# Kernel optimization log

Measured on AMD Instinct MI355X. Metric: run time of the kernel, lower is better.

The kernel has to match this reference:

```python
import jax, jax.numpy as jnp
import numpy as np

B, S, H = 32, 4096, 512


def setup_inputs() -> dict:
    key = jax.random.key(0)
    k1, k2, k3, k4, k5 = jax.random.split(key, 5)
    scale = 1.0 / np.sqrt(H)
    return {
        "query": jax.random.normal(k1, (B, H), dtype=jnp.float32),
        "keys": jax.random.normal(k2, (B, S, H), dtype=jnp.float32),
        "key_mask": jnp.ones((B, S), dtype=bool),
        "Wq": jax.random.uniform(k3, (H, H), jnp.float32, -scale, scale),
        "Wk": jax.random.uniform(k4, (H, H), jnp.float32, -scale, scale),
        "v": jax.random.uniform(k5, (H,), jnp.float32, -scale, scale),
    }


def reference(query, keys, key_mask, Wq, Wk, v):
    # Additive (Bahdanau) attention.
    # nn.Linear(x) = x @ W.T
    q = query @ Wq.T                       # [B, H]
    k = keys @ Wk.T                        # [B, S, H]
    scores = jnp.einsum('bsh,h->bs', jnp.tanh(q[:, None, :] + k), v)  # [B, S]
    scores = jnp.where(key_mask, scores, -1e9)
    attn = jax.nn.softmax(scores, axis=-1)  # [B, S]
    ctx = jnp.einsum('bs,bsh->bh', attn, keys)  # [B, H]
    return (ctx, attn)
```

## Files before the change

### kernel.cpp

```cpp
#include <hip/hip_runtime.h>
#include <hip/hip_bf16.h>
#include <cstdint>

#define B_ 32
#define S_ 4096
#define H_ 512

typedef _Float16 f16x8 __attribute__((ext_vector_type(8)));
typedef _Float16 f16x4 __attribute__((ext_vector_type(4)));
typedef float    f32x4 __attribute__((ext_vector_type(4)));

__device__ __forceinline__ float tanh_fast(float x) {
    float e = __expf(2.0f * x);
    return 1.0f - 2.0f / (e + 1.0f);
}

__global__ void prep_q(const float* __restrict__ query,
                       const float* __restrict__ Wq,
                       float* __restrict__ q_ws) {
    int b = blockIdx.x;
    int t = threadIdx.x;
    __shared__ float qs[H_];
    qs[t]       = query[b * H_ + t];
    qs[t + 256] = query[b * H_ + t + 256];
    __syncthreads();
    for (int ii = 0; ii < 2; ++ii) {
        int i = t + ii * 256;
        const float4* wrow = (const float4*)(Wq + (size_t)i * H_);
        float acc = 0.f;
        #pragma unroll 8
        for (int h4 = 0; h4 < H_ / 4; ++h4) {
            float4 w = wrow[h4];
            acc += qs[h4*4+0]*w.x + qs[h4*4+1]*w.y + qs[h4*4+2]*w.z + qs[h4*4+3]*w.w;
        }
        q_ws[b * H_ + i] = acc;
    }
}

__global__ void prep_wk(const float* __restrict__ Wk, _Float16* __restrict__ wk16) {
    int tid = blockIdx.x * 256 + threadIdx.x;
    int c  = tid & 3;
    int i  = (tid >> 2) & 511;
    int ks = tid >> 11;
    const float* src = Wk + (size_t)i * H_ + ks * 32 + c * 8;
    float4 a = *(const float4*)(src);
    float4 d = *(const float4*)(src + 4);
    f16x8 p;
    p[0] = (_Float16)a.x; p[1] = (_Float16)a.y; p[2] = (_Float16)a.z; p[3] = (_Float16)a.w;
    p[4] = (_Float16)d.x; p[5] = (_Float16)d.y; p[6] = (_Float16)d.z; p[7] = (_Float16)d.w;
    int swz = c ^ ((i >> 1) & 3);
    *(f16x8*)(wk16 + (size_t)ks * 16384 + i * 32 + swz * 8) = p;
}

__global__ __launch_bounds__(256, 2) void scores_kernel(
        const float* __restrict__ keys, const _Float16* __restrict__ wk16,
        const float* __restrict__ q_ws, const float* __restrict__ v,
        float* __restrict__ scores) {
    __shared__ __align__(16) _Float16 As[64 * 32];
    __shared__ __align__(16) _Float16 Bs[512 * 32];
    __shared__ float srow[4][64];

    int t    = threadIdx.x;
    int lane = t & 63;
    int wid  = t >> 6;
    int m0   = blockIdx.x * 64;
    int b    = m0 >> 12;

    f32x4 acc[4][8] = {};

    for (int ks = 0; ks < 16; ++ks) {
        __syncthreads();
        #pragma unroll
        for (int r2 = 0; r2 < 2; ++r2) {
            int idx = t + r2 * 256;
            int row = idx >> 3, c4 = idx & 7;
            float4 kv = *(const float4*)(keys + (size_t)(m0 + row) * H_ + ks * 32 + c4 * 4);
            f16x4 h;
            h[0] = (_Float16)kv.x; h[1] = (_Float16)kv.y;
            h[2] = (_Float16)kv.z; h[3] = (_Float16)kv.w;
            int chunk = c4 >> 1;
            int swz = chunk ^ ((row >> 1) & 3);
            *(f16x4*)&As[row * 32 + swz * 8 + (c4 & 1) * 4] = h;
        }
        {
            const uint4* bsrc = (const uint4*)(wk16 + (size_t)ks * 16384);
            uint4* bdst = (uint4*)Bs;
            #pragma unroll
            for (int j = 0; j < 8; ++j)
                bdst[t + j * 256] = bsrc[t + j * 256];
        }
        __syncthreads();
        int chunk = lane >> 4;
        f16x8 af[4];
        #pragma unroll
        for (int mf = 0; mf < 4; ++mf) {
            int row = mf * 16 + (lane & 15);
            af[mf] = *(const f16x8*)&As[row * 32 + (chunk ^ ((row >> 1) & 3)) * 8];
        }
        f16x8 bf[8];
        #pragma unroll
        for (int nf = 0; nf < 8; ++nf) {
            int row = wid * 128 + nf * 16 + (lane & 15);
            bf[nf] = *(const f16x8*)&Bs[row * 32 + (chunk ^ ((row >> 1) & 3)) * 8];
        }
        #pragma unroll
        for (int mf = 0; mf < 4; ++mf)
            #pragma unroll
            for (int nf = 0; nf < 8; ++nf)
                acc[mf][nf] = __builtin_amdgcn_mfma_f32_16x16x32_f16(af[mf], bf[nf], acc[mf][nf], 0, 0, 0);
    }

    float qv[8], vv[8];
    #pragma unroll
    for (int nf = 0; nf < 8; ++nf) {
        int col = wid * 128 + nf * 16 + (lane & 15);
        qv[nf] = q_ws[b * H_ + col];
        vv[nf] = v[col];
    }
    #pragma unroll
    for (int mf = 0; mf < 4; ++mf) {
        f32x4 rs = {0.f, 0.f, 0.f, 0.f};
        #pragma unroll
        for (int nf = 0; nf < 8; ++nf)
            #pragma unroll
            for (int r = 0; r < 4; ++r)
                rs[r] += tanh_fast(qv[nf] + acc[mf][nf][r]) * vv[nf];
        #pragma unroll
        for (int off = 1; off < 16; off <<= 1)
            #pragma unroll
            for (int r = 0; r < 4; ++r)
                rs[r] += __shfl_xor(rs[r], off);
        if ((lane & 15) == 0) {
            #pragma unroll
            for (int r = 0; r < 4; ++r)
                srow[wid][mf * 16 + (lane >> 4) * 4 + r] = rs[r];
        }
    }
    __syncthreads();
    if (t < 64)
        scores[m0 + t] = srow[0][t] + srow[1][t] + srow[2][t] + srow[3][t];
}

__global__ void softmax_kernel(const float* __restrict__ scores,
                               const int* __restrict__ mask,
                               float* __restrict__ attn) {
    int b = blockIdx.x, t = threadIdx.x;
    __shared__ float red[8];
    float x[16];
    float m = -1e30f;
    #pragma unroll
    for (int j = 0; j < 16; ++j) {
        int s = t + j * 256;
        float sc = scores[b * S_ + s];
        x[j] = (mask[b * S_ + s] != 0) ? sc : -1e9f;
        m = fmaxf(m, x[j]);
    }
    #pragma unroll
    for (int off = 1; off < 64; off <<= 1) m = fmaxf(m, __shfl_xor(m, off));
    if ((t & 63) == 0) red[t >> 6] = m;
    __syncthreads();
    m = fmaxf(fmaxf(red[0], red[1]), fmaxf(red[2], red[3]));
    float sum = 0.f;
    #pragma unroll
    for (int j = 0; j < 16; ++j) { x[j] = __expf(x[j] - m); sum += x[j]; }
    #pragma unroll
    for (int off = 1; off < 64; off <<= 1) sum += __shfl_xor(sum, off);
    if ((t & 63) == 0) red[4 + (t >> 6)] = sum;
    __syncthreads();
    float inv = 1.0f / (red[4] + red[5] + red[6] + red[7]);
    #pragma unroll
    for (int j = 0; j < 16; ++j)
        attn[b * S_ + t + j * 256] = x[j] * inv;
}

__global__ void ctx_kernel(const float* __restrict__ keys,
                           const float* __restrict__ attn,
                           float* __restrict__ ctx) {
    int blk = blockIdx.x;
    int b = blk >> 4, c = blk & 15;
    int s0 = c * 256;
    int t = threadIdx.x;
    __shared__ float attn_s[256];
    __shared__ float ctx_l[512];
    attn_s[t] = attn[b * S_ + s0 + t];
    __syncthreads();
    int h4 = t & 127, sp = t >> 7;
    f32x4 acc = {0.f, 0.f, 0.f, 0.f};
    const float4* kb = (const float4*)(keys + ((size_t)b * S_ + s0) * H_);
    for (int it = 0; it < 128; ++it) {
        int srow = it * 2 + sp;
        float a = attn_s[srow];
        float4 kv = kb[(size_t)srow * 128 + h4];
        acc[0] += a * kv.x; acc[1] += a * kv.y; acc[2] += a * kv.z; acc[3] += a * kv.w;
    }
    if (sp == 0) {
        #pragma unroll
        for (int r = 0; r < 4; ++r) ctx_l[h4 * 4 + r] = acc[r];
    }
    __syncthreads();
    if (sp == 1) {
        #pragma unroll
        for (int r = 0; r < 4; ++r) ctx_l[h4 * 4 + r] += acc[r];
    }
    __syncthreads();
    atomicAdd(&ctx[b * H_ + t], ctx_l[t]);
    atomicAdd(&ctx[b * H_ + t + 256], ctx_l[t + 256]);
}

extern "C" void kernel_launch(void* const* d_in, const int* in_sizes, int n_in,
                              void* d_out, int out_size, void* d_ws, size_t ws_size,
                              hipStream_t stream) {
    const float* query = (const float*)d_in[0];
    const float* keys  = (const float*)d_in[1];
    const int*   mask  = (const int*)d_in[2];
    const float* Wq    = (const float*)d_in[3];
    const float* Wk    = (const float*)d_in[4];
    const float* v     = (const float*)d_in[5];

    float* out  = (float*)d_out;
    float* ctx  = out;
    float* attn = out + B_ * H_;

    char* ws = (char*)d_ws;
    float*    q_ws   = (float*)ws;
    _Float16* wk16   = (_Float16*)(ws + 65536);
    float*    scores = (float*)(ws + 65536 + 524288);

    hipMemsetAsync(ctx, 0, B_ * H_ * sizeof(float), stream);
    prep_q<<<32, 256, 0, stream>>>(query, Wq, q_ws);
    prep_wk<<<128, 256, 0, stream>>>(Wk, wk16);
    scores_kernel<<<2048, 256, 0, stream>>>(keys, wk16, q_ws, v, scores);
    softmax_kernel<<<32, 256, 0, stream>>>(scores, mask, attn);
    ctx_kernel<<<512, 256, 0, stream>>>(keys, attn, ctx);
}
```

Measured before the change: 489.5 us.

## Double-buffer scores GEMM tiles with direct global-to-LDS loads; parallelize prep_q

The scores kernel now double-buffers its A and B LDS tiles. The next Wk slice is prefetched with global_load_lds directly into shared memory, and the next keys slice is loaded into registers while the current MFMAs run. This removes one barrier per k-step and overlaps global latency with compute, at the cost of doubling LDS use to about 66KB, which may limit the 2-blocks-per-CU occupancy target. prep_q is also split across 256 blocks, with four threads per output row and a shuffle reduction, to fix its poor parallelism.

```diff
diff --git a/kernel.cpp b/kernel.cpp
--- a/kernel.cpp
+++ b/kernel.cpp
@@ -10,6 +10,10 @@
 typedef _Float16 f16x4 __attribute__((ext_vector_type(4)));
 typedef float    f32x4 __attribute__((ext_vector_type(4)));
 
+#define GLDS16(gsrc, ldst) \
+    __builtin_amdgcn_global_load_lds((const __attribute__((address_space(1))) void*)(gsrc), \
+        (__attribute__((address_space(3))) void*)(ldst), 16, 0, 0)
+
 __device__ __forceinline__ float tanh_fast(float x) {
     float e = __expf(2.0f * x);
     return 1.0f - 2.0f / (e + 1.0f);
@@ -18,23 +22,27 @@
 __global__ void prep_q(const float* __restrict__ query,
                        const float* __restrict__ Wq,
                        float* __restrict__ q_ws) {
-    int b = blockIdx.x;
-    int t = threadIdx.x;
+    int blk = blockIdx.x;
+    int b   = blk >> 3;
+    int r0  = (blk & 7) * 64;
+    int t   = threadIdx.x;
     __shared__ float qs[H_];
     qs[t]       = query[b * H_ + t];
     qs[t + 256] = query[b * H_ + t + 256];
     __syncthreads();
-    for (int ii = 0; ii < 2; ++ii) {
-        int i = t + ii * 256;
-        const float4* wrow = (const float4*)(Wq + (size_t)i * H_);
-        float acc = 0.f;
-        #pragma unroll 8
-        for (int h4 = 0; h4 < H_ / 4; ++h4) {
-            float4 w = wrow[h4];
-            acc += qs[h4*4+0]*w.x + qs[h4*4+1]*w.y + qs[h4*4+2]*w.z + qs[h4*4+3]*w.w;
-        }
-        q_ws[b * H_ + i] = acc;
-    }
+    int row  = r0 + (t >> 2);
+    int part = t & 3;
+    const float4* wrow = (const float4*)(Wq + (size_t)row * H_) + part * 32;
+    const float*  qsp  = qs + part * 128;
+    float acc = 0.f;
+    #pragma unroll 8
+    for (int j = 0; j < 32; ++j) {
+        float4 w = wrow[j];
+        acc += qsp[j*4+0]*w.x + qsp[j*4+1]*w.y + qsp[j*4+2]*w.z + qsp[j*4+3]*w.w;
+    }
+    acc += __shfl_xor(acc, 1);
+    acc += __shfl_xor(acc, 2);
+    if (part == 0) q_ws[b * H_ + row] = acc;
 }
 
 __global__ void prep_wk(const float* __restrict__ Wk, _Float16* __restrict__ wk16) {
@@ -56,8 +64,8 @@
         const float* __restrict__ keys, const _Float16* __restrict__ wk16,
         const float* __restrict__ q_ws, const float* __restrict__ v,
         float* __restrict__ scores) {
-    __shared__ __align__(16) _Float16 As[64 * 32];
-    __shared__ __align__(16) _Float16 Bs[512 * 32];
+    __shared__ __align__(16) _Float16 As[2][64 * 32];
+    __shared__ __align__(16) _Float16 Bs[2][512 * 32];
     __shared__ float srow[4][64];
 
     int t    = threadIdx.x;
@@ -65,49 +73,69 @@
     int wid  = t >> 6;
     int m0   = blockIdx.x * 64;
     int b    = m0 >> 12;
+    const float* akeys = keys + (size_t)m0 * H_;
 
     f32x4 acc[4][8] = {};
 
+    int arow0 = t >> 3, ac4 = t & 7;
+    int arow1 = arow0 + 32;
+    int aswz0 = (ac4 >> 1) ^ ((arow0 >> 1) & 3);
+    int aswz1 = (ac4 >> 1) ^ ((arow1 >> 1) & 3);
+
+    {
+        const _Float16* bsrc = wk16;
+        #pragma unroll
+        for (int j = 0; j < 8; ++j)
+            GLDS16(bsrc + (j * 256 + t) * 8, &Bs[0][(j * 256 + t) * 8]);
+        float4 kv0 = *(const float4*)(akeys + (size_t)arow0 * H_ + ac4 * 4);
+        float4 kv1 = *(const float4*)(akeys + (size_t)arow1 * H_ + ac4 * 4);
+        f16x4 h0, h1;
+        h0[0] = (_Float16)kv0.x; h0[1] = (_Float16)kv0.y; h0[2] = (_Float16)kv0.z; h0[3] = (_Float16)kv0.w;
+        h1[0] = (_Float16)kv1.x; h1[1] = (_Float16)kv1.y; h1[2] = (_Float16)kv1.z; h1[3] = (_Float16)kv1.w;
+        *(f16x4*)&As[0][arow0 * 32 + aswz0 * 8 + (ac4 & 1) * 4] = h0;
+        *(f16x4*)&As[0][arow1 * 32 + aswz1 * 8 + (ac4 & 1) * 4] = h1;
+    }
+    __syncthreads();
+
+    int cur = 0;
     for (int ks = 0; ks < 16; ++ks) {
-        __syncthreads();
-        #pragma unroll
-        for (int r2 = 0; r2 < 2; ++r2) {
-            int idx = t + r2 * 256;
-            int row = idx >> 3, c4 = idx & 7;
-            float4 kv = *(const float4*)(keys + (size_t)(m0 + row) * H_ + ks * 32 + c4 * 4);
-            f16x4 h;
-            h[0] = (_Float16)kv.x; h[1] = (_Float16)kv.y;
-            h[2] = (_Float16)kv.z; h[3] = (_Float16)kv.w;
-            int chunk = c4 >> 1;
-            int swz = chunk ^ ((row >> 1) & 3);
-            *(f16x4*)&As[row * 32 + swz * 8 + (c4 & 1) * 4] = h;
-        }
-        {
-            const uint4* bsrc = (const uint4*)(wk16 + (size_t)ks * 16384);
-            uint4* bdst = (uint4*)Bs;
+        int nb = cur ^ 1;
+        float4 kv0, kv1;
+        if (ks < 15) {
+            const _Float16* bsrc = wk16 + (size_t)(ks + 1) * 16384;
             #pragma unroll
             for (int j = 0; j < 8; ++j)
-                bdst[t + j * 256] = bsrc[t + j * 256];
-        }
-        __syncthreads();
+                GLDS16(bsrc + (j * 256 + t) * 8, &Bs[nb][(j * 256 + t) * 8]);
+            kv0 = *(const float4*)(akeys + (size_t)arow0 * H_ + (ks + 1) * 32 + ac4 * 4);
+            kv1 = *(const float4*)(akeys + (size_t)arow1 * H_ + (ks + 1) * 32 + ac4 * 4);
+        }
         int chunk = lane >> 4;
         f16x8 af[4];
         #pragma unroll
         for (int mf = 0; mf < 4; ++mf) {
             int row = mf * 16 + (lane & 15);
-            af[mf] = *(const f16x8*)&As[row * 32 + (chunk ^ ((row >> 1) & 3)) * 8];
+            af[mf] = *(const f16x8*)&As[cur][row * 32 + (chunk ^ ((row >> 1) & 3)) * 8];
         }
         f16x8 bf[8];
         #pragma unroll
         for (int nf = 0; nf < 8; ++nf) {
             int row = wid * 128 + nf * 16 + (lane & 15);
-            bf[nf] = *(const f16x8*)&Bs[row * 32 + (chunk ^ ((row >> 1) & 3)) * 8];
+            bf[nf] = *(const f16x8*)&Bs[cur][row * 32 + (chunk ^ ((row >> 1) & 3)) * 8];
         }
         #pragma unroll
         for (int mf = 0; mf < 4; ++mf)
             #pragma unroll
             for (int nf = 0; nf < 8; ++nf)
                 acc[mf][nf] = __builtin_amdgcn_mfma_f32_16x16x32_f16(af[mf], bf[nf], acc[mf][nf], 0, 0, 0);
+        if (ks < 15) {
+            f16x4 h0, h1;
+            h0[0] = (_Float16)kv0.x; h0[1] = (_Float16)kv0.y; h0[2] = (_Float16)kv0.z; h0[3] = (_Float16)kv0.w;
+            h1[0] = (_Float16)kv1.x; h1[1] = (_Float16)kv1.y; h1[2] = (_Float16)kv1.z; h1[3] = (_Float16)kv1.w;
+            *(f16x4*)&As[nb][arow0 * 32 + aswz0 * 8 + (ac4 & 1) * 4] = h0;
+            *(f16x4*)&As[nb][arow1 * 32 + aswz1 * 8 + (ac4 & 1) * 4] = h1;
+        }
+        __syncthreads();
+        cur = nb;
     }
 
     float qv[8], vv[8];
@@ -227,7 +255,7 @@
     float*    scores = (float*)(ws + 65536 + 524288);
 
     hipMemsetAsync(ctx, 0, B_ * H_ * sizeof(float), stream);
-    prep_q<<<32, 256, 0, stream>>>(query, Wq, q_ws);
+    prep_q<<<256, 256, 0, stream>>>(query, Wq, q_ws);
     prep_wk<<<128, 256, 0, stream>>>(Wk, wk16);
     scores_kernel<<<2048, 256, 0, stream>>>(keys, wk16, q_ws, v, scores);
     softmax_kernel<<<32, 256, 0, stream>>>(scores, mask, attn);
```

Result: no change. 494.6 us (+1.0%).
